# Performance work log

Hardware: AMD Instinct MI355X
Metric: run time of the kernel (lower is better)

## Reference

```python
import jax, jax.numpy as jnp
import numpy as np

N_HEADS = 16


def setup_inputs() -> dict:
    key = jax.random.key(0)
    ks = jax.random.split(key, 5)
    B, S, D = 2, 2048, 1024
    x = jax.random.normal(ks[0], (B, S, D), dtype=jnp.float32)
    Wqkv = jax.random.normal(ks[1], (D, 3 * D), dtype=jnp.float32) * (1.0 / np.sqrt(D))
    bqkv = jax.random.normal(ks[2], (3 * D,), dtype=jnp.float32) * 0.02
    Wout = jax.random.normal(ks[3], (D, D), dtype=jnp.float32) * (1.0 / np.sqrt(D))
    bout = jax.random.normal(ks[4], (D,), dtype=jnp.float32) * 0.02
    return {"x": x, "Wqkv": Wqkv, "bqkv": bqkv, "Wout": Wout, "bout": bout}


def reference(x, Wqkv, bqkv, Wout, bout):
    B, S, D = x.shape
    H = N_HEADS
    dh = D // H
    # qkv projection, then view as [B,S,H,3*dh] and chunk on last dim
    # (matches torch: per-head q/k/v are interleaved slices of the projection)
    qkv = (x @ Wqkv + bqkv).reshape(B, S, H, 3 * dh).transpose(0, 2, 1, 3)  # [B,H,S,3dh]
    q, k, v = jnp.split(qkv, 3, axis=-1)  # each [B,H,S,dh]
    scale = jnp.asarray(1.0 / np.sqrt(dh), dtype=x.dtype)
    scores = jnp.einsum('bhqd,bhkd->bhqk', q, k) * scale  # [B,H,S,S]
    causal = jnp.tril(jnp.ones((S, S), dtype=bool))
    scores = jnp.where(causal, scores, jnp.asarray(-jnp.inf, dtype=scores.dtype))
    attn_w = jax.nn.softmax(scores, axis=-1)
    attn = jnp.einsum('bhqk,bhkd->bhqd', attn_w, v)  # [B,H,S,dh]
    attn = attn.transpose(0, 2, 1, 3).reshape(B, S, D)
    return attn @ Wout + bout
```

## Files before the change

### kernel.cpp

```cpp
#include <hip/hip_runtime.h>
#include <hip/hip_bf16.h>
#include <cstdint>
#include <cstddef>

typedef __hip_bfloat16 bf16;
typedef short bf16x4 __attribute__((ext_vector_type(4)));
typedef short bf16x8 __attribute__((ext_vector_type(8)));
typedef float f32x4 __attribute__((ext_vector_type(4)));

#define LOG2E 1.44269504088896f

static constexpr int Bb = 2, S = 2048, D = 1024, H = 16, DH = 64;

__device__ inline short f2bf_bits(float f) {
  bf16 b = __float2bfloat16(f);
  short s;
  __builtin_memcpy(&s, &b, 2);
  return s;
}
__device__ inline float bfbits2f(short s) {
  uint32_t u = ((uint32_t)(uint16_t)s) << 16;
  float f;
  __builtin_memcpy(&f, &u, 4);
  return f;
}

__global__ __launch_bounds__(256) void prep_kernel(
    const float* __restrict__ Wqkv, bf16* __restrict__ wqkvT,
    const float* __restrict__ Wout, bf16* __restrict__ woutT,
    const float* __restrict__ x, bf16* __restrict__ xbf) {
  const int blk = blockIdx.x;
  const int tid = threadIdx.x;
  if (blk < 4096) {
    __shared__ float t[32][33];
    const float* in;
    bf16* out;
    int R, C, bx, by;
    if (blk < 3072) { in = Wqkv; out = wqkvT; R = 1024; C = 3072; bx = blk % 96; by = blk / 96; }
    else            { in = Wout; out = woutT; R = 1024; C = 1024; bx = (blk - 3072) % 32; by = (blk - 3072) / 32; }
    int c0 = bx * 32, r0 = by * 32;
    int tx = tid & 31, ty = tid >> 5;
#pragma unroll
    for (int i = 0; i < 4; i++) {
      int r = ty + i * 8;
      t[r][tx] = in[(size_t)(r0 + r) * C + c0 + tx];
    }
    __syncthreads();
#pragma unroll
    for (int i = 0; i < 4; i++) {
      int c = ty + i * 8;
      out[(size_t)(c0 + c) * R + r0 + tx] = __float2bfloat16(t[tx][c]);
    }
  } else {
    size_t i = ((size_t)(blk - 4096) * 256 + tid) * 8;
    f32x4 a = *(const f32x4*)(x + i);
    f32x4 b = *(const f32x4*)(x + i + 4);
    bf16x8 v;
#pragma unroll
    for (int j = 0; j < 4; j++) { v[j] = f2bf_bits(a[j]); v[4 + j] = f2bf_bits(b[j]); }
    *(bf16x8*)((short*)xbf + i) = v;
  }
}

__global__ __launch_bounds__(256) void gemm_qkv(
    const bf16* __restrict__ A, const bf16* __restrict__ Bt,
    const float* __restrict__ bias,
    bf16* __restrict__ Qb, bf16* __restrict__ Kb, bf16* __restrict__ Vtb) {
  constexpr int K = 1024;
  __shared__ __align__(16) short smA[128 * 32];
  __shared__ __align__(16) short smB[128 * 32];
  __shared__ __align__(16) short smE[4][16 * 72];

  const int tid = threadIdx.x;
  const int wave = tid >> 6, lane = tid & 63;
  const int quad = lane >> 4, l16 = lane & 15;
  const int m0 = blockIdx.y * 128, n0 = blockIdx.x * 128;
  const int wm = wave >> 1, wn = wave & 1;

  f32x4 acc[4][4];
#pragma unroll
  for (int i = 0; i < 4; i++)
#pragma unroll
    for (int j = 0; j < 4; j++) acc[i][j] = {0.f, 0.f, 0.f, 0.f};

  const int srow = lane >> 2;
  const int scol = (lane & 3) * 8;

  for (int k0 = 0; k0 < K; k0 += 32) {
#pragma unroll
    for (int half = 0; half < 2; half++) {
      int row = half * 64 + wave * 16 + srow;
      const bf16* ga = A + (size_t)(m0 + row) * K + k0 + scol;
      const bf16* gb = Bt + (size_t)(n0 + row) * K + k0 + scol;
      __builtin_amdgcn_global_load_lds(
          (const __attribute__((address_space(1))) void*)ga,
          (__attribute__((address_space(3))) void*)&smA[(half * 64 + wave * 16) * 32],
          16, 0, 0);
      __builtin_amdgcn_global_load_lds(
          (const __attribute__((address_space(1))) void*)gb,
          (__attribute__((address_space(3))) void*)&smB[(half * 64 + wave * 16) * 32],
          16, 0, 0);
    }
    __syncthreads();

    bf16x8 af[4], bf_[4];
#pragma unroll
    for (int mi = 0; mi < 4; mi++)
      af[mi] = *(const bf16x8*)&smA[(wm * 64 + mi * 16 + l16) * 32 + quad * 8];
#pragma unroll
    for (int ni = 0; ni < 4; ni++)
      bf_[ni] = *(const bf16x8*)&smB[(wn * 64 + ni * 16 + l16) * 32 + quad * 8];
#pragma unroll
    for (int mi = 0; mi < 4; mi++)
#pragma unroll
      for (int ni = 0; ni < 4; ni++)
        acc[mi][ni] = __builtin_amdgcn_mfma_f32_16x16x32_bf16(
            af[mi], bf_[ni], acc[mi][ni], 0, 0, 0);
    __syncthreads();
  }

  const int cs0 = n0 + wn * 64;
  const int h = cs0 / 192;
  const int rt = (cs0 >> 6) % 3;
  const int t0w = m0 + wm * 64;
  const int b = t0w >> 11, s0w = t0w & 2047;

  float bv[4];
#pragma unroll
  for (int ni = 0; ni < 4; ni++) bv[ni] = bias[cs0 + ni * 16 + l16];

  if (rt < 2) {
    bf16* dst = (rt == 0 ? Qb : Kb) + ((size_t)(b * H + h) * S + s0w) * 64;
    short* sE = &smE[wave][0];
    const int r8 = lane >> 2, s4 = lane & 3;
#pragma unroll
    for (int mi = 0; mi < 4; mi++) {
#pragma unroll
      for (int ni = 0; ni < 4; ni++)
#pragma unroll
        for (int r = 0; r < 4; r++)
          sE[(quad * 4 + r) * 72 + ni * 16 + l16] = f2bf_bits(acc[mi][ni][r] + bv[ni]);
      asm volatile("s_waitcnt lgkmcnt(0)" ::: "memory");
      bf16x8 w0 = *(const bf16x8*)&sE[r8 * 72 + s4 * 16];
      bf16x8 w1 = *(const bf16x8*)&sE[r8 * 72 + s4 * 16 + 8];
      short* g = (short*)dst + (size_t)(mi * 16 + r8) * 64 + s4 * 16;
      *(bf16x8*)g = w0;
      *(bf16x8*)(g + 8) = w1;
      asm volatile("s_waitcnt lgkmcnt(0)" ::: "memory");
    }
  } else {
#pragma unroll
    for (int ni = 0; ni < 4; ni++) {
      const int dh = ni * 16 + l16;
#pragma unroll
      for (int mi = 0; mi < 4; mi++) {
        const int s0 = s0w + mi * 16 + quad * 4;
        size_t base = ((size_t)(b * H + h) * 64 + dh) * S + s0;
        bf16x4 vv;
#pragma unroll
        for (int r = 0; r < 4; r++) vv[r] = f2bf_bits(acc[mi][ni][r] + bv[ni]);
        *(bf16x4*)((short*)Vtb + base) = vv;
      }
    }
  }
}

__global__ __launch_bounds__(256) void gemm_out(
    const bf16* __restrict__ A, const bf16* __restrict__ Bt,
    const float* __restrict__ bias, float* __restrict__ C,
    int M, int N, int K) {
  constexpr int BN = 64, NF = 2;
  __shared__ __align__(16) short smA[128 * 32];
  __shared__ __align__(16) short smB[BN * 32];
  __shared__ __align__(16) float smEf[4][580];

  const int tid = threadIdx.x;
  const int wave = tid >> 6, lane = tid & 63;
  const int quad = lane >> 4, l16 = lane & 15;
  const int m0 = blockIdx.y * 128, n0 = blockIdx.x * BN;
  const int wm = wave >> 1, wn = wave & 1;

  f32x4 acc[4][NF];
#pragma unroll
  for (int i = 0; i < 4; i++)
#pragma unroll
    for (int j = 0; j < NF; j++) acc[i][j] = {0.f, 0.f, 0.f, 0.f};

  const int srow = lane >> 2;
  const int scol = (lane & 3) * 8;

  for (int k0 = 0; k0 < K; k0 += 32) {
#pragma unroll
    for (int half = 0; half < 2; half++) {
      int row = half * 64 + wave * 16 + srow;
      const bf16* ga = A + (size_t)(m0 + row) * K + k0 + scol;
      __builtin_amdgcn_global_load_lds(
          (const __attribute__((address_space(1))) void*)ga,
          (__attribute__((address_space(3))) void*)&smA[(half * 64 + wave * 16) * 32],
          16, 0, 0);
    }
    {
      int row = wave * 16 + srow;
      const bf16* gb = Bt + (size_t)(n0 + row) * K + k0 + scol;
      __builtin_amdgcn_global_load_lds(
          (const __attribute__((address_space(1))) void*)gb,
          (__attribute__((address_space(3))) void*)&smB[(wave * 16) * 32],
          16, 0, 0);
    }
    __syncthreads();

    bf16x8 af[4], bf_[NF];
#pragma unroll
    for (int mi = 0; mi < 4; mi++)
      af[mi] = *(const bf16x8*)&smA[(wm * 64 + mi * 16 + l16) * 32 + quad * 8];
#pragma unroll
    for (int ni = 0; ni < NF; ni++)
      bf_[ni] = *(const bf16x8*)&smB[(wn * 32 + ni * 16 + l16) * 32 + quad * 8];
#pragma unroll
    for (int mi = 0; mi < 4; mi++)
#pragma unroll
      for (int ni = 0; ni < NF; ni++)
        acc[mi][ni] = __builtin_amdgcn_mfma_f32_16x16x32_bf16(
            af[mi], bf_[ni], acc[mi][ni], 0, 0, 0);
    __syncthreads();
  }

  float bv[NF];
#pragma unroll
  for (int ni = 0; ni < NF; ni++) bv[ni] = bias[n0 + wn * 32 + ni * 16 + l16];

  float* sE = &smEf[wave][0];
#pragma unroll
  for (int mi = 0; mi < 4; mi++) {
#pragma unroll
    for (int ni = 0; ni < NF; ni++)
#pragma unroll
      for (int r = 0; r < 4; r++)
        sE[(quad * 4 + r) * 36 + ni * 16 + l16] = acc[mi][ni][r] + bv[ni];
    asm volatile("s_waitcnt lgkmcnt(0)" ::: "memory");
#pragma unroll
    for (int t = 0; t < 2; t++) {
      int slot = t * 64 + lane;
      int rr = slot >> 3, c4 = slot & 7;
      f32x4 v = *(const f32x4*)&sE[rr * 36 + c4 * 4];
      int row = m0 + wm * 64 + mi * 16 + rr;
      int col = n0 + wn * 32 + c4 * 4;
      *(f32x4*)&C[(size_t)row * N + col] = v;
    }
    asm volatile("s_waitcnt lgkmcnt(0)" ::: "memory");
  }
}

__global__ __launch_bounds__(256) void attn_kernel(
    const bf16* __restrict__ Qb, const bf16* __restrict__ Kb,
    const bf16* __restrict__ Vtb,
    bf16* __restrict__ Op0, bf16* __restrict__ Op1,
    float* __restrict__ lp0, float* __restrict__ lp1,
    bf16* __restrict__ Ofinal, int split) {
  const int blk = blockIdx.x;
  int sk, p, bh;
  if (split == 2) { sk = blk & 1; p = (blk >> 1) & 15; bh = blk >> 5; }
  else            { sk = 0;       p = blk & 15;        bh = blk >> 4; }
  const int h = bh & (H - 1), b = bh >> 4;
  const int tid = threadIdx.x;
  const int wave = tid >> 6, lane = tid & 63;
  const int quad = lane >> 4, l16 = lane & 15;

  bf16* __restrict__ Op = sk ? Op1 : Op0;
  float* __restrict__ lp = sk ? lp1 : lp0;

  const bf16* Qh = Qb + (size_t)(b * H + h) * S * 64;
  const bf16* Kh = Kb + (size_t)(b * H + h) * S * 64;
  const bf16* Vth = Vtb + (size_t)(b * H + h) * 64 * S;

  __shared__ __align__(16) short smK[64 * 64];
  __shared__ __align__(16) short smVt[64 * 64];
  __shared__ __align__(16) short pLds[4][16][76];

  const int lrow = lane >> 3;
  const int lg = lane & 7;
  const float PSCALE = 0.125f * LOG2E;
  const int swz = l16 & 7;

#pragma unroll
  for (int pass = 0; pass < 2; pass++) {
    const int qt = pass ? p : (31 - p);
    const int q0 = qt * 64 + wave * 16;
    const int qglob = q0 + l16;

    bf16x8 aQ[2];
#pragma unroll
    for (int kh = 0; kh < 2; kh++)
      aQ[kh] = *(const bf16x8*)(Qh + (size_t)(q0 + l16) * 64 + kh * 32 + quad * 8);

    f32x4 o[4];
#pragma unroll
    for (int dt = 0; dt < 4; dt++) o[dt] = {0.f, 0.f, 0.f, 0.f};
    float lsum = 0.f;

    for (int it = sk; it <= qt; it += split) {
      const int kv0 = it * 64;
      __syncthreads();

#pragma unroll
      for (int j = 0; j < 2; j++) {
        const int row = wave * 16 + j * 8 + lrow;
        const bf16* ks = Kh + (size_t)(kv0 + row) * 64 + (lg ^ (row & 7)) * 8;
        __builtin_amdgcn_global_load_lds(
            (const __attribute__((address_space(1))) void*)ks,
            (__attribute__((address_space(3))) void*)&smK[(wave * 16 + j * 8) * 64],
            16, 0, 0);
        const bf16* vs = Vth + (size_t)row * S + kv0 + (lg ^ (row & 7)) * 8;
        __builtin_amdgcn_global_load_lds(
            (const __attribute__((address_space(1))) void*)vs,
            (__attribute__((address_space(3))) void*)&smVt[(wave * 16 + j * 8) * 64],
            16, 0, 0);
      }
      __syncthreads();

      f32x4 z[4];
#pragma unroll
      for (int nh = 0; nh < 4; nh++) {
        const int row = nh * 16 + l16;
        f32x4 t = {0.f, 0.f, 0.f, 0.f};
#pragma unroll
        for (int kh = 0; kh < 2; kh++) {
          bf16x8 bK = *(const bf16x8*)&smK[row * 64 + ((kh * 4 + quad) ^ swz) * 8];
          t = __builtin_amdgcn_mfma_f32_16x16x32_bf16(bK, aQ[kh], t, 0, 0, 0);
        }
        z[nh] = t;
      }

      const bool full = (it < qt);

#pragma unroll
      for (int nh = 0; nh < 4; nh++) {
        const int kbase = kv0 + nh * 16 + quad * 4;
        bf16x4 pk;
        float lacc = 0.f;
#pragma unroll
        for (int r = 0; r < 4; r++) {
          float e = exp2f(z[nh][r] * PSCALE);
          e = (full || (kbase + r <= qglob)) ? e : 0.f;
          lacc += e;
          pk[r] = f2bf_bits(e);
        }
        lsum += lacc;
        *(bf16x4*)&pLds[wave][l16][nh * 16 + quad * 4] = pk;
      }

      asm volatile("s_waitcnt lgkmcnt(0)" ::: "memory");

      bf16x8 aP[2];
#pragma unroll
      for (int k2 = 0; k2 < 2; k2++)
        aP[k2] = *(const bf16x8*)&pLds[wave][l16][k2 * 32 + quad * 8];
#pragma unroll
      for (int dt = 0; dt < 4; dt++) {
        const int row = dt * 16 + l16;
#pragma unroll
        for (int k2 = 0; k2 < 2; k2++) {
          bf16x8 bV = *(const bf16x8*)&smVt[row * 64 + ((k2 * 4 + quad) ^ swz) * 8];
          o[dt] = __builtin_amdgcn_mfma_f32_16x16x32_bf16(aP[k2], bV, o[dt], 0, 0, 0);
        }
      }
    }

    float l = lsum;
    l += __shfl_xor(l, 16, 64);
    l += __shfl_xor(l, 32, 64);

    if (split == 2) {
      const size_t rowbase = (size_t)(b * H + h) * S + q0;
      if (quad == 0) lp[rowbase + l16] = l;
#pragma unroll
      for (int r = 0; r < 4; r++) {
        const size_t row = rowbase + quad * 4 + r;
#pragma unroll
        for (int dt = 0; dt < 4; dt++)
          ((short*)Op)[row * 64 + dt * 16 + l16] = f2bf_bits(o[dt][r]);
      }
    } else {
#pragma unroll
      for (int r = 0; r < 4; r++) {
        const float lr = __shfl(l, quad * 4 + r, 64);
        const float inv = 1.f / lr;
        const int q = q0 + quad * 4 + r;
#pragma unroll
        for (int dt = 0; dt < 4; dt++)
          Ofinal[(size_t)(b * S + q) * D + h * 64 + dt * 16 + l16] =
              __float2bfloat16(o[dt][r] * inv);
      }
    }
  }
}

__global__ __launch_bounds__(256) void attn_reduce(
    const bf16* __restrict__ O0, const bf16* __restrict__ O1,
    const float* __restrict__ l0, const float* __restrict__ l1,
    bf16* __restrict__ attnO) {
  int gid = blockIdx.x * 256 + threadIdx.x;
  int row = gid >> 3;
  int c8 = (gid & 7) * 8;
  float inv = 1.f / (l0[row] + l1[row]);
  bf16x8 a = *(const bf16x8*)((const short*)O0 + (size_t)row * 64 + c8);
  bf16x8 bb = *(const bf16x8*)((const short*)O1 + (size_t)row * 64 + c8);
  bf16x8 o;
#pragma unroll
  for (int j = 0; j < 8; j++)
    o[j] = f2bf_bits((bfbits2f(a[j]) + bfbits2f(bb[j])) * inv);
  int bh = row >> 11, q = row & 2047;
  int b = bh >> 4, h = bh & 15;
  *(bf16x8*)((short*)attnO + (((size_t)(b * S + q) * H + h) * 64 + c8)) = o;
}

extern "C" void kernel_launch(void* const* d_in, const int* in_sizes, int n_in,
                              void* d_out, int out_size, void* d_ws, size_t ws_size,
                              hipStream_t stream) {
  const float* x    = (const float*)d_in[0];
  const float* Wqkv = (const float*)d_in[1];
  const float* bqkv = (const float*)d_in[2];
  const float* Wout = (const float*)d_in[3];
  const float* bout = (const float*)d_in[4];
  float* out = (float*)d_out;

  char* ws = (char*)d_ws;
  const bool split2 = (ws_size >= 50855936);

  bf16* Qb  = (bf16*)(ws);
  bf16* Kb  = (bf16*)(ws + 8388608);
  bf16* Vtb = (bf16*)(ws + 16777216);
  bf16* xbf = (bf16*)(ws + 25165824);

  bf16 *Op0, *Op1, *attnO;
  float *lp0, *lp1;
  bf16 *wqkvT, *woutT;
  if (split2) {
    Op0   = (bf16*)(ws + 25165824);
    Op1   = (bf16*)(ws + 33554432);
    lp0   = (float*)(ws + 41943040);
    lp1   = (float*)(ws + 42205184);
    attnO = (bf16*)(ws + 8388608);
    wqkvT = (bf16*)(ws + 42467328);
    woutT = (bf16*)(ws + 48758784);
  } else {
    Op0 = Op1 = nullptr; lp0 = lp1 = nullptr;
    attnO = (bf16*)(ws + 25165824);
    wqkvT = (bf16*)(ws + 33554432);
    woutT = (bf16*)(ws + 39845888);
  }

  prep_kernel<<<dim3(6144), 256, 0, stream>>>(Wqkv, wqkvT, Wout, woutT, x, xbf);

  gemm_qkv<<<dim3(3072 / 128, 4096 / 128), 256, 0, stream>>>(
      xbf, wqkvT, bqkv, Qb, Kb, Vtb);

  if (split2) {
    attn_kernel<<<dim3(1024), 256, 0, stream>>>(
        Qb, Kb, Vtb, Op0, Op1, lp0, lp1, nullptr, 2);
    attn_reduce<<<dim3(2048), 256, 0, stream>>>(Op0, Op1, lp0, lp1, attnO);
  } else {
    attn_kernel<<<dim3(512), 256, 0, stream>>>(
        Qb, Kb, Vtb, nullptr, nullptr, nullptr, nullptr, attnO, 1);
  }

  gemm_out<<<dim3(1024 / 64, 4096 / 128), 256, 0, stream>>>(
      attnO, woutT, bout, out, 4096, 1024, 1024);
}
```

Measured before the change: 190.7 us.

## Add three-way KV split, fold softmax scale into Q, MFMA row sums

Adds a split-3 attention path over KV tiles, with a three-input reduce, chosen when the workspace is large enough. The softmax scale is folded into Q during the QKV projection epilogue, and the per-row exp sum is accumulated with an MFMA against ones instead of scalar adds and shuffles. The causal mask check is compiled only into the diagonal tile. These aim to balance causal work across more blocks and cut ALU work in the inner loop, at the cost of more partial-output traffic and an extra MFMA per tile.

```diff
diff --git a/kernel.cpp b/kernel.cpp
--- a/kernel.cpp
+++ b/kernel.cpp
@@ -11,6 +11,9 @@
 #define LOG2E 1.44269504088896f
 
 static constexpr int Bb = 2, S = 2048, D = 1024, H = 16, DH = 64;
+
+struct TrueT  { static constexpr bool value = true;  };
+struct FalseT { static constexpr bool value = false; };
 
 __device__ inline short f2bf_bits(float f) {
   bf16 b = __float2bfloat16(f);
@@ -130,6 +133,7 @@
   for (int ni = 0; ni < 4; ni++) bv[ni] = bias[cs0 + ni * 16 + l16];
 
   if (rt < 2) {
+    const float qscale = (rt == 0) ? (0.125f * LOG2E) : 1.0f;
     bf16* dst = (rt == 0 ? Qb : Kb) + ((size_t)(b * H + h) * S + s0w) * 64;
     short* sE = &smE[wave][0];
     const int r8 = lane >> 2, s4 = lane & 3;
@@ -139,7 +143,8 @@
       for (int ni = 0; ni < 4; ni++)
 #pragma unroll
         for (int r = 0; r < 4; r++)
-          sE[(quad * 4 + r) * 72 + ni * 16 + l16] = f2bf_bits(acc[mi][ni][r] + bv[ni]);
+          sE[(quad * 4 + r) * 72 + ni * 16 + l16] =
+              f2bf_bits((acc[mi][ni][r] + bv[ni]) * qscale);
       asm volatile("s_waitcnt lgkmcnt(0)" ::: "memory");
       bf16x8 w0 = *(const bf16x8*)&sE[r8 * 72 + s4 * 16];
       bf16x8 w1 = *(const bf16x8*)&sE[r8 * 72 + s4 * 16 + 8];
@@ -254,20 +259,21 @@
 __global__ __launch_bounds__(256) void attn_kernel(
     const bf16* __restrict__ Qb, const bf16* __restrict__ Kb,
     const bf16* __restrict__ Vtb,
-    bf16* __restrict__ Op0, bf16* __restrict__ Op1,
-    float* __restrict__ lp0, float* __restrict__ lp1,
+    bf16* __restrict__ Op0, bf16* __restrict__ Op1, bf16* __restrict__ Op2,
+    float* __restrict__ lp0, float* __restrict__ lp1, float* __restrict__ lp2,
     bf16* __restrict__ Ofinal, int split) {
   const int blk = blockIdx.x;
   int sk, p, bh;
-  if (split == 2) { sk = blk & 1; p = (blk >> 1) & 15; bh = blk >> 5; }
-  else            { sk = 0;       p = blk & 15;        bh = blk >> 4; }
+  if (split == 3)      { sk = blk % 3; int r = blk / 3; p = r & 15; bh = r >> 4; }
+  else if (split == 2) { sk = blk & 1; p = (blk >> 1) & 15; bh = blk >> 5; }
+  else                 { sk = 0;       p = blk & 15;        bh = blk >> 4; }
   const int h = bh & (H - 1), b = bh >> 4;
   const int tid = threadIdx.x;
   const int wave = tid >> 6, lane = tid & 63;
   const int quad = lane >> 4, l16 = lane & 15;
 
-  bf16* __restrict__ Op = sk ? Op1 : Op0;
-  float* __restrict__ lp = sk ? lp1 : lp0;
+  bf16*  __restrict__ Op = (sk == 0) ? Op0 : (sk == 1) ? Op1 : Op2;
+  float* __restrict__ lp = (sk == 0) ? lp0 : (sk == 1) ? lp1 : lp2;
 
   const bf16* Qh = Qb + (size_t)(b * H + h) * S * 64;
   const bf16* Kh = Kb + (size_t)(b * H + h) * S * 64;
@@ -279,8 +285,11 @@
 
   const int lrow = lane >> 3;
   const int lg = lane & 7;
-  const float PSCALE = 0.125f * LOG2E;
   const int swz = l16 & 7;
+
+  bf16x8 onesB;
+#pragma unroll
+  for (int j = 0; j < 8; j++) onesB[j] = (short)0x3F80;
 
 #pragma unroll
   for (int pass = 0; pass < 2; pass++) {
@@ -296,9 +305,10 @@
     f32x4 o[4];
 #pragma unroll
     for (int dt = 0; dt < 4; dt++) o[dt] = {0.f, 0.f, 0.f, 0.f};
-    float lsum = 0.f;
-
-    for (int it = sk; it <= qt; it += split) {
+    f32x4 lacc = {0.f, 0.f, 0.f, 0.f};
+
+    auto tile = [&](int it, auto diag_tag) {
+      constexpr bool DIAG = decltype(diag_tag)::value;
       const int kv0 = it * 64;
       __syncthreads();
 
@@ -331,21 +341,18 @@
         z[nh] = t;
       }
 
-      const bool full = (it < qt);
-
 #pragma unroll
       for (int nh = 0; nh < 4; nh++) {
-        const int kbase = kv0 + nh * 16 + quad * 4;
         bf16x4 pk;
-        float lacc = 0.f;
 #pragma unroll
         for (int r = 0; r < 4; r++) {
-          float e = exp2f(z[nh][r] * PSCALE);
-          e = (full || (kbase + r <= qglob)) ? e : 0.f;
-          lacc += e;
+          float e = exp2f(z[nh][r]);
+          if (DIAG) {
+            const int kidx = kv0 + nh * 16 + quad * 4 + r;
+            e = (kidx <= qglob) ? e : 0.f;
+          }
           pk[r] = f2bf_bits(e);
         }
-        lsum += lacc;
         *(bf16x4*)&pLds[wave][l16][nh * 16 + quad * 4] = pk;
       }
 
@@ -355,6 +362,9 @@
 #pragma unroll
       for (int k2 = 0; k2 < 2; k2++)
         aP[k2] = *(const bf16x8*)&pLds[wave][l16][k2 * 32 + quad * 8];
+#pragma unroll
+      for (int k2 = 0; k2 < 2; k2++)
+        lacc = __builtin_amdgcn_mfma_f32_16x16x32_bf16(aP[k2], onesB, lacc, 0, 0, 0);
 #pragma unroll
       for (int dt = 0; dt < 4; dt++) {
         const int row = dt * 16 + l16;
@@ -364,15 +374,18 @@
           o[dt] = __builtin_amdgcn_mfma_f32_16x16x32_bf16(aP[k2], bV, o[dt], 0, 0, 0);
         }
       }
-    }
-
-    float l = lsum;
-    l += __shfl_xor(l, 16, 64);
-    l += __shfl_xor(l, 32, 64);
-
-    if (split == 2) {
+    };
+
+    int it = sk;
+    for (; it < qt; it += split) tile(it, FalseT{});
+    if (it == qt) tile(qt, TrueT{});
+
+    if (split > 1) {
       const size_t rowbase = (size_t)(b * H + h) * S + q0;
-      if (quad == 0) lp[rowbase + l16] = l;
+      if (l16 == 0) {
+#pragma unroll
+        for (int r = 0; r < 4; r++) lp[rowbase + quad * 4 + r] = lacc[r];
+      }
 #pragma unroll
       for (int r = 0; r < 4; r++) {
         const size_t row = rowbase + quad * 4 + r;
@@ -383,8 +396,7 @@
     } else {
 #pragma unroll
       for (int r = 0; r < 4; r++) {
-        const float lr = __shfl(l, quad * 4 + r, 64);
-        const float inv = 1.f / lr;
+        const float inv = 1.f / lacc[r];
         const int q = q0 + quad * 4 + r;
 #pragma unroll
         for (int dt = 0; dt < 4; dt++)
@@ -397,18 +409,29 @@
 
 __global__ __launch_bounds__(256) void attn_reduce(
     const bf16* __restrict__ O0, const bf16* __restrict__ O1,
+    const bf16* __restrict__ O2,
     const float* __restrict__ l0, const float* __restrict__ l1,
-    bf16* __restrict__ attnO) {
+    const float* __restrict__ l2,
+    bf16* __restrict__ attnO, int nparts) {
   int gid = blockIdx.x * 256 + threadIdx.x;
   int row = gid >> 3;
   int c8 = (gid & 7) * 8;
-  float inv = 1.f / (l0[row] + l1[row]);
+  float lsum = l0[row] + l1[row];
+  if (nparts == 3) lsum += l2[row];
+  float inv = 1.f / lsum;
   bf16x8 a = *(const bf16x8*)((const short*)O0 + (size_t)row * 64 + c8);
   bf16x8 bb = *(const bf16x8*)((const short*)O1 + (size_t)row * 64 + c8);
+  float acc[8];
+#pragma unroll
+  for (int j = 0; j < 8; j++) acc[j] = bfbits2f(a[j]) + bfbits2f(bb[j]);
+  if (nparts == 3) {
+    bf16x8 c = *(const bf16x8*)((const short*)O2 + (size_t)row * 64 + c8);
+#pragma unroll
+    for (int j = 0; j < 8; j++) acc[j] += bfbits2f(c[j]);
+  }
   bf16x8 o;
 #pragma unroll
-  for (int j = 0; j < 8; j++)
-    o[j] = f2bf_bits((bfbits2f(a[j]) + bfbits2f(bb[j])) * inv);
+  for (int j = 0; j < 8; j++) o[j] = f2bf_bits(acc[j] * inv);
   int bh = row >> 11, q = row & 2047;
   int b = bh >> 4, h = bh & 15;
   *(bf16x8*)((short*)attnO + (((size_t)(b * S + q) * H + h) * 64 + c8)) = o;
@@ -425,17 +448,30 @@
   float* out = (float*)d_out;
 
   char* ws = (char*)d_ws;
-  const bool split2 = (ws_size >= 50855936);
+  int split;
+  if (ws_size >= 59506688)      split = 3;
+  else if (ws_size >= 50855936) split = 2;
+  else                          split = 1;
 
   bf16* Qb  = (bf16*)(ws);
   bf16* Kb  = (bf16*)(ws + 8388608);
   bf16* Vtb = (bf16*)(ws + 16777216);
   bf16* xbf = (bf16*)(ws + 25165824);
 
-  bf16 *Op0, *Op1, *attnO;
-  float *lp0, *lp1;
+  bf16 *Op0 = nullptr, *Op1 = nullptr, *Op2 = nullptr, *attnO;
+  float *lp0 = nullptr, *lp1 = nullptr, *lp2 = nullptr;
   bf16 *wqkvT, *woutT;
-  if (split2) {
+  if (split == 3) {
+    Op0   = (bf16*)(ws + 25165824);
+    Op1   = (bf16*)(ws + 33554432);
+    Op2   = (bf16*)(ws + 41943040);
+    lp0   = (float*)(ws + 50331648);
+    lp1   = (float*)(ws + 50593792);
+    lp2   = (float*)(ws + 50855936);
+    attnO = (bf16*)(ws + 8388608);
+    wqkvT = (bf16*)(ws + 51118080);
+    woutT = (bf16*)(ws + 57409536);
+  } else if (split == 2) {
     Op0   = (bf16*)(ws + 25165824);
     Op1   = (bf16*)(ws + 33554432);
     lp0   = (float*)(ws + 41943040);
@@ -444,7 +480,6 @@
     wqkvT = (bf16*)(ws + 42467328);
     woutT = (bf16*)(ws + 48758784);
   } else {
-    Op0 = Op1 = nullptr; lp0 = lp1 = nullptr;
     attnO = (bf16*)(ws + 25165824);
     wqkvT = (bf16*)(ws + 33554432);
     woutT = (bf16*)(ws + 39845888);
@@ -455,13 +490,17 @@
   gemm_qkv<<<dim3(3072 / 128, 4096 / 128), 256, 0, stream>>>(
       xbf, wqkvT, bqkv, Qb, Kb, Vtb);
 
-  if (split2) {
+  if (split == 3) {
+    attn_kernel<<<dim3(1536), 256, 0, stream>>>(
+        Qb, Kb, Vtb, Op0, Op1, Op2, lp0, lp1, lp2, nullptr, 3);
+    attn_reduce<<<dim3(2048), 256, 0, stream>>>(Op0, Op1, Op2, lp0, lp1, lp2, attnO, 3);
+  } else if (split == 2) {
     attn_kernel<<<dim3(1024), 256, 0, stream>>>(
-        Qb, Kb, Vtb, Op0, Op1, lp0, lp1, nullptr, 2);
-    attn_reduce<<<dim3(2048), 256, 0, stream>>>(Op0, Op1, lp0, lp1, attnO);
+        Qb, Kb, Vtb, Op0, Op1, Op0, lp0, lp1, lp0, nullptr, 2);
+    attn_reduce<<<dim3(2048), 256, 0, stream>>>(Op0, Op1, Op0, lp0, lp1, lp0, attnO, 2);
   } else {
     attn_kernel<<<dim3(512), 256, 0, stream>>>(
-        Qb, Kb, Vtb, nullptr, nullptr, nullptr, nullptr, attnO, 1);
+        Qb, Kb, Vtb, nullptr, nullptr, nullptr, nullptr, nullptr, nullptr, attnO, 1);
   }
 
   gemm_out<<<dim3(1024 / 64, 4096 / 128), 256, 0, stream>>>(
```

Result: no change. 192.3 us (+0.9%).
